# Optimization experiments

Hardware: AMD Instinct MI355X
Metric: run time of the kernel (lower is better)

Reference implementation:

```python
import jax, jax.numpy as jnp
import numpy as np

N_NODES = 65536
N_EDGES = 1048576
IN_F = 128
HID_F = 128
OUT_F = 128


def setup_inputs() -> dict:
    key = jax.random.key(0)
    ks = jax.random.split(key, 8)
    feat = jax.random.normal(ks[0], (N_NODES, IN_F), dtype=jnp.float32)
    eweight = jax.random.uniform(ks[1], (N_EDGES, 1), dtype=jnp.float32)
    W1 = jax.random.normal(ks[2], (IN_F, HID_F), dtype=jnp.float32) * (1.0 / np.sqrt(IN_F))
    b1 = jnp.zeros((HID_F,), dtype=jnp.float32)
    W2 = jax.random.normal(ks[3], (HID_F, OUT_F), dtype=jnp.float32) * (1.0 / np.sqrt(HID_F))
    b2 = jnp.zeros((OUT_F,), dtype=jnp.float32)
    src = jax.random.randint(ks[4], (N_EDGES,), 0, N_NODES, dtype=jnp.int32)
    dst = jax.random.randint(ks[5], (N_EDGES,), 0, N_NODES, dtype=jnp.int32)
    return {"feat": feat, "eweight": eweight, "W1": W1, "b1": b1,
            "W2": W2, "b2": b2, "src": src, "dst": dst}


def _degrees(src, dst, n_nodes):
    ones = jnp.ones(src.shape[0], dtype=jnp.float32)
    deg_out = jax.ops.segment_sum(ones, src, num_segments=n_nodes)
    deg_in = jax.ops.segment_sum(ones, dst, num_segments=n_nodes)
    # DGL GraphConv clamps degree to min 1 before norm='both'
    return jnp.clip(deg_out, 1.0, None), jnp.clip(deg_in, 1.0, None)


def _graph_conv(feat, W, b, src, dst, out_norm, in_norm, n_nodes):
    # DGL GraphConv, norm='both': D_out^{-1/2} x -> x W -> spmm sum -> D_in^{-1/2} -> + b
    h = feat * out_norm[:, None]
    h = h @ W
    agg = jax.ops.segment_sum(h[src], dst, num_segments=n_nodes)
    return agg * in_norm[:, None] + b


def reference(feat, eweight, W1, b1, W2, b2, src, dst):
    n = feat.shape[0]
    deg_out, deg_in = _degrees(src, dst, n)
    out_norm = jax.lax.rsqrt(deg_out)
    in_norm = jax.lax.rsqrt(deg_in)
    h = _graph_conv(feat, W1, b1, src, dst, out_norm, in_norm, n)
    h = jax.nn.relu(h)
    h = _graph_conv(h, W2, b2, src, dst, out_norm, in_norm, n)
    # final update_all: u_mul_e + sum (eweight given)
    msg = h[src] * eweight  # [E, OUT_F]
    return jax.ops.segment_sum(msg, dst, num_segments=n)
```

## Files before the change

### kernel.cpp

```cpp
#include <hip/hip_runtime.h>

#define F 128
#define NBA 512
#define COARSE 256
#define CAP_BIN 4864
#define CAP_CSR 5632

typedef unsigned int uint;
typedef unsigned short ushort;
typedef unsigned char uchar;
typedef __attribute__((ext_vector_type(8))) short short8;
typedef __attribute__((ext_vector_type(8))) unsigned short ushort8;
typedef __attribute__((ext_vector_type(4))) float floatx4;

__device__ __forceinline__ ushort f2bf(float f) {
  uint u = __float_as_uint(f);
  u += 0x7fffu + ((u >> 16) & 1u);
  return (ushort)(u >> 16);
}

__global__ __launch_bounds__(256) void w_prep(const float* __restrict__ W1,
                                              const float* __restrict__ W2,
                                              ushort* __restrict__ W1t,
                                              ushort* __restrict__ W2t) {
  int b = blockIdx.x;
  const float* W = (b < 64) ? W1 : W2;
  ushort* Wt = (b < 64) ? W1t : W2t;
  int idx = (b & 63) * 256 + threadIdx.x;
  int k = idx >> 7, n = idx & 127;
  Wt[n * F + k] = f2bf(W[idx]);
}

__global__ void init_cursors(int* __restrict__ cursorD, int* __restrict__ cursorS) {
  int t = threadIdx.x;
  cursorD[t] = t * CAP_BIN;
  cursorS[t] = t * CAP_BIN;
}

__global__ __launch_bounds__(256) void bin_edges(
    const int* __restrict__ src, const int* __restrict__ dst,
    const float* __restrict__ ew, int E,
    int* __restrict__ cursorD, int* __restrict__ cursorS,
    uchar* __restrict__ dstKeyF, uint* __restrict__ payload, uchar* __restrict__ srcF) {
  __shared__ int cnt[COARSE];
  __shared__ int base[COARSE];
  bool isD = blockIdx.x < NBA;
  int blk = isD ? blockIdx.x : blockIdx.x - NBA;
  const int* key = isD ? dst : src;
  int* cursor = isD ? cursorD : cursorS;
  if (threadIdx.x < COARSE) cnt[threadIdx.x] = 0;
  __syncthreads();
  int chunk = (E + NBA - 1) / NBA;
  int s0 = blk * chunk, s1 = min(E, s0 + chunk);
  for (int i = s0 + threadIdx.x; i < s1; i += 256)
    atomicAdd(&cnt[key[i] >> 8], 1);
  __syncthreads();
  if (threadIdx.x < COARSE) {
    int c = cnt[threadIdx.x];
    base[threadIdx.x] = c ? atomicAdd(&cursor[threadIdx.x], c) : 0;
    cnt[threadIdx.x] = 0;
  }
  __syncthreads();
  if (isD) {
    for (int i = s0 + threadIdx.x; i < s1; i += 256) {
      int d = dst[i];
      int bin = d >> 8;
      int p = base[bin] + atomicAdd(&cnt[bin], 1);
      if (p < (bin + 1) * CAP_BIN) {
        dstKeyF[p] = (uchar)(d & 255);
        payload[p] = (uint)(src[i] & 0xffff) | ((uint)f2bf(ew[i]) << 16);
      }
    }
  } else {
    for (int i = s0 + threadIdx.x; i < s1; i += 256) {
      int s = src[i];
      int bin = s >> 8;
      int p = base[bin] + atomicAdd(&cnt[bin], 1);
      if (p < (bin + 1) * CAP_BIN) srcF[p] = (uchar)(s & 255);
    }
  }
}

__global__ __launch_bounds__(1024) void bucket_csr(
    const uchar* __restrict__ dstKeyF, const uint* __restrict__ payload,
    const int* __restrict__ cursorD, int2* __restrict__ rowRange,
    float* __restrict__ inNorm, uint* __restrict__ csr,
    const uchar* __restrict__ srcF, const int* __restrict__ cursorS,
    float* __restrict__ outNorm) {
  __shared__ int hist[256], base[256], cur[256];
  int b = blockIdx.x, t = threadIdx.x;
  int lo = b * CAP_BIN;
  int cntD = min(cursorD[b] - lo, CAP_BIN);
  int hi = lo + cntD;
  if (t < 256) hist[t] = 0;
  __syncthreads();
  for (int i = lo + t; i < hi; i += 1024)
    atomicAdd(&hist[dstKeyF[i]], 1);
  __syncthreads();
  if (t < 256) base[t] = (hist[t] + 3) & ~3;
  __syncthreads();
  for (int off = 1; off < 256; off <<= 1) {
    int x = 0;
    if (t < 256 && t >= off) x = base[t - off];
    __syncthreads();
    if (t < 256) base[t] += x;
    __syncthreads();
  }
  if (t < 256) {
    int v = hist[t];
    int sz4 = (v + 3) & ~3;
    int st = b * CAP_CSR + base[t] - sz4;
    base[t] = st;
    cur[t] = 0;
    int node = b * 256 + t;
    rowRange[node] = make_int2(st, v);
    inNorm[node] = rsqrtf((float)max(v, 1));
  }
  __syncthreads();
  for (int i = lo + t; i < hi; i += 1024) {
    int fine = dstKeyF[i];
    int p = base[fine] + atomicAdd(&cur[fine], 1);
    csr[p] = payload[i];
  }
  __syncthreads();
  if (t < 256) hist[t] = 0;
  __syncthreads();
  int cntS = min(cursorS[b] - lo, CAP_BIN);
  for (int i = lo + t; i < lo + cntS; i += 1024)
    atomicAdd(&hist[srcF[i]], 1);
  __syncthreads();
  if (t < 256) outNorm[b * 256 + t] = rsqrtf((float)max(hist[t], 1));
}


template <bool BF16IN>
__global__ __launch_bounds__(256) void gemm_mfma(
    const void* __restrict__ Xv, const float* __restrict__ scale,
    const ushort* __restrict__ Wt, ushort* __restrict__ Y) {
  __shared__ ushort sA[128 * 136];
  __shared__ ushort sB[128 * 136];
  int t = threadIdx.x;
  int row0 = blockIdx.x * 128;

  {
    int r = t >> 1, hf = t & 1;
    ushort* ap = sA + r * 136 + hf * 64;
    if (BF16IN) {
      const ushort* xp = (const ushort*)Xv + (size_t)(row0 + r) * F + hf * 64;
#pragma unroll
      for (int j = 0; j < 8; ++j)
        *(ushort8*)(ap + j * 8) = *(const ushort8*)(xp + j * 8);
    } else {
      const float* xp = (const float*)Xv + (size_t)(row0 + r) * F + hf * 64;
      float s = scale[row0 + r];
#pragma unroll
      for (int j = 0; j < 8; ++j) {
        float4 v0 = *(const float4*)(xp + j * 8);
        float4 v1 = *(const float4*)(xp + j * 8 + 4);
        ushort8 o;
        o[0] = f2bf(v0.x * s); o[1] = f2bf(v0.y * s); o[2] = f2bf(v0.z * s); o[3] = f2bf(v0.w * s);
        o[4] = f2bf(v1.x * s); o[5] = f2bf(v1.y * s); o[6] = f2bf(v1.z * s); o[7] = f2bf(v1.w * s);
        *(ushort8*)(ap + j * 8) = o;
      }
    }
  }
  {
    int n = t >> 1, hf = t & 1;
    const ushort* wp = Wt + n * F + hf * 64;
    ushort* bp = sB + n * 136 + hf * 64;
#pragma unroll
    for (int j = 0; j < 8; ++j)
      *(ushort8*)(bp + j * 8) = *(const ushort8*)(wp + j * 8);
  }
  __syncthreads();

  int lane = t & 63, wave = t >> 6;
  int quad = lane >> 4, l16 = lane & 15;
  int mrow0 = wave * 32;

  floatx4 acc[2][8];
#pragma unroll
  for (int a = 0; a < 2; ++a)
#pragma unroll
    for (int c = 0; c < 8; ++c) acc[a][c] = (floatx4){0.f, 0.f, 0.f, 0.f};

#pragma unroll
  for (int kc = 0; kc < 128; kc += 32) {
    short8 afrag[2], bfrag[8];
#pragma unroll
    for (int a = 0; a < 2; ++a)
      afrag[a] = *(const short8*)(sA + (mrow0 + a * 16 + l16) * 136 + kc + quad * 8);
#pragma unroll
    for (int c = 0; c < 8; ++c)
      bfrag[c] = *(const short8*)(sB + (c * 16 + l16) * 136 + kc + quad * 8);
#pragma unroll
    for (int a = 0; a < 2; ++a)
#pragma unroll
      for (int c = 0; c < 8; ++c)
        acc[a][c] = __builtin_amdgcn_mfma_f32_16x16x32_bf16(afrag[a], bfrag[c], acc[a][c], 0, 0, 0);
  }

#pragma unroll
  for (int a = 0; a < 2; ++a)
#pragma unroll
    for (int c = 0; c < 8; ++c)
#pragma unroll
      for (int r = 0; r < 4; ++r) {
        int row = row0 + mrow0 + a * 16 + quad * 4 + r;
        int col = c * 16 + l16;
        Y[(size_t)row * F + col] = f2bf(acc[a][c][r]);
      }
}


template <bool EW, bool NB, bool RELU, bool PS, bool OUT_BF16>
__global__ __launch_bounds__(256) void spmm(
    const ushort* __restrict__ hb, const int2* __restrict__ rowRange,
    const uint* __restrict__ csr, const float* __restrict__ inNorm,
    const float* __restrict__ bias, const float* __restrict__ postScale,
    void* __restrict__ outv) {
  int node = blockIdx.x * 4 + (threadIdx.x >> 6);
  int lane = threadIdx.x & 63;
  int2 rr = rowRange[node];
  int base = rr.x, len = rr.y;

  float ax0 = 0.f, ay0 = 0.f, ax1 = 0.f, ay1 = 0.f;
  float ax2 = 0.f, ay2 = 0.f, ax3 = 0.f, ay3 = 0.f;
  int i = 0;
  for (; i + 8 <= len; i += 8) {
    uint4 c0 = *(const uint4*)(csr + base + i);
    uint4 c1 = *(const uint4*)(csr + base + i + 4);
    uint e0 = c0.x, e1 = c0.y, e2 = c0.z, e3 = c0.w;
    uint e4 = c1.x, e5 = c1.y, e6 = c1.z, e7 = c1.w;
    uint w0 = *((const uint*)(hb + ((size_t)(e0 & 0xffffu) << 7)) + lane);
    uint w1 = *((const uint*)(hb + ((size_t)(e1 & 0xffffu) << 7)) + lane);
    uint w2 = *((const uint*)(hb + ((size_t)(e2 & 0xffffu) << 7)) + lane);
    uint w3 = *((const uint*)(hb + ((size_t)(e3 & 0xffffu) << 7)) + lane);
    uint w4 = *((const uint*)(hb + ((size_t)(e4 & 0xffffu) << 7)) + lane);
    uint w5 = *((const uint*)(hb + ((size_t)(e5 & 0xffffu) << 7)) + lane);
    uint w6 = *((const uint*)(hb + ((size_t)(e6 & 0xffffu) << 7)) + lane);
    uint w7 = *((const uint*)(hb + ((size_t)(e7 & 0xffffu) << 7)) + lane);
    if (EW) {
      float q0 = __uint_as_float(e0 & 0xffff0000u), q1 = __uint_as_float(e1 & 0xffff0000u);
      float q2 = __uint_as_float(e2 & 0xffff0000u), q3 = __uint_as_float(e3 & 0xffff0000u);
      float q4 = __uint_as_float(e4 & 0xffff0000u), q5 = __uint_as_float(e5 & 0xffff0000u);
      float q6 = __uint_as_float(e6 & 0xffff0000u), q7 = __uint_as_float(e7 & 0xffff0000u);
      ax0 = fmaf(__uint_as_float(w0 << 16), q0, ax0); ay0 = fmaf(__uint_as_float(w0 & 0xffff0000u), q0, ay0);
      ax1 = fmaf(__uint_as_float(w1 << 16), q1, ax1); ay1 = fmaf(__uint_as_float(w1 & 0xffff0000u), q1, ay1);
      ax2 = fmaf(__uint_as_float(w2 << 16), q2, ax2); ay2 = fmaf(__uint_as_float(w2 & 0xffff0000u), q2, ay2);
      ax3 = fmaf(__uint_as_float(w3 << 16), q3, ax3); ay3 = fmaf(__uint_as_float(w3 & 0xffff0000u), q3, ay3);
      ax0 = fmaf(__uint_as_float(w4 << 16), q4, ax0); ay0 = fmaf(__uint_as_float(w4 & 0xffff0000u), q4, ay0);
      ax1 = fmaf(__uint_as_float(w5 << 16), q5, ax1); ay1 = fmaf(__uint_as_float(w5 & 0xffff0000u), q5, ay1);
      ax2 = fmaf(__uint_as_float(w6 << 16), q6, ax2); ay2 = fmaf(__uint_as_float(w6 & 0xffff0000u), q6, ay2);
      ax3 = fmaf(__uint_as_float(w7 << 16), q7, ax3); ay3 = fmaf(__uint_as_float(w7 & 0xffff0000u), q7, ay3);
    } else {
      ax0 += __uint_as_float(w0 << 16) + __uint_as_float(w4 << 16);
      ay0 += __uint_as_float(w0 & 0xffff0000u) + __uint_as_float(w4 & 0xffff0000u);
      ax1 += __uint_as_float(w1 << 16) + __uint_as_float(w5 << 16);
      ay1 += __uint_as_float(w1 & 0xffff0000u) + __uint_as_float(w5 & 0xffff0000u);
      ax2 += __uint_as_float(w2 << 16) + __uint_as_float(w6 << 16);
      ay2 += __uint_as_float(w2 & 0xffff0000u) + __uint_as_float(w6 & 0xffff0000u);
      ax3 += __uint_as_float(w3 << 16) + __uint_as_float(w7 << 16);
      ay3 += __uint_as_float(w3 & 0xffff0000u) + __uint_as_float(w7 & 0xffff0000u);
    }
  }
  if (i + 4 <= len) {
    uint4 c = *(const uint4*)(csr + base + i);
    uint e0 = c.x, e1 = c.y, e2 = c.z, e3 = c.w;
    uint w0 = *((const uint*)(hb + ((size_t)(e0 & 0xffffu) << 7)) + lane);
    uint w1 = *((const uint*)(hb + ((size_t)(e1 & 0xffffu) << 7)) + lane);
    uint w2 = *((const uint*)(hb + ((size_t)(e2 & 0xffffu) << 7)) + lane);
    uint w3 = *((const uint*)(hb + ((size_t)(e3 & 0xffffu) << 7)) + lane);
    float q0 = EW ? __uint_as_float(e0 & 0xffff0000u) : 1.f;
    float q1 = EW ? __uint_as_float(e1 & 0xffff0000u) : 1.f;
    float q2 = EW ? __uint_as_float(e2 & 0xffff0000u) : 1.f;
    float q3 = EW ? __uint_as_float(e3 & 0xffff0000u) : 1.f;
    ax0 = fmaf(__uint_as_float(w0 << 16), q0, ax0); ay0 = fmaf(__uint_as_float(w0 & 0xffff0000u), q0, ay0);
    ax1 = fmaf(__uint_as_float(w1 << 16), q1, ax1); ay1 = fmaf(__uint_as_float(w1 & 0xffff0000u), q1, ay1);
    ax2 = fmaf(__uint_as_float(w2 << 16), q2, ax2); ay2 = fmaf(__uint_as_float(w2 & 0xffff0000u), q2, ay2);
    ax3 = fmaf(__uint_as_float(w3 << 16), q3, ax3); ay3 = fmaf(__uint_as_float(w3 & 0xffff0000u), q3, ay3);
    i += 4;
  }
  int r = len - i;
  if (r > 0) {
    uint4 c = *(const uint4*)(csr + base + i);
    uint ee[4] = {c.x, c.y, c.z, c.w};
#pragma unroll
    for (int j = 0; j < 3; ++j) {
      if (j < r) {
        uint wj = *((const uint*)(hb + ((size_t)(ee[j] & 0xffffu) << 7)) + lane);
        float q = EW ? __uint_as_float(ee[j] & 0xffff0000u) : 1.f;
        if (j == 0) { ax0 = fmaf(__uint_as_float(wj << 16), q, ax0); ay0 = fmaf(__uint_as_float(wj & 0xffff0000u), q, ay0); }
        if (j == 1) { ax1 = fmaf(__uint_as_float(wj << 16), q, ax1); ay1 = fmaf(__uint_as_float(wj & 0xffff0000u), q, ay1); }
        if (j == 2) { ax2 = fmaf(__uint_as_float(wj << 16), q, ax2); ay2 = fmaf(__uint_as_float(wj & 0xffff0000u), q, ay2); }
      }
    }
  }
  float rx = (ax0 + ax1) + (ax2 + ax3);
  float ry = (ay0 + ay1) + (ay2 + ay3);
  if (NB) {
    float sc = inNorm[node];
    float2 b = *((const float2*)bias + lane);
    rx = fmaf(rx, sc, b.x);
    ry = fmaf(ry, sc, b.y);
    if (RELU) { rx = fmaxf(rx, 0.f); ry = fmaxf(ry, 0.f); }
    if (PS) { float o = postScale[node]; rx *= o; ry *= o; }
  }
  if (OUT_BF16) {
    uint p = ((uint)f2bf(ry) << 16) | (uint)f2bf(rx);
    *((uint*)outv + ((size_t)node << 6) + lane) = p;
  } else {
    float2 rv = {rx, ry};
    *((float2*)outv + ((size_t)node << 6) + lane) = rv;
  }
}


extern "C" void kernel_launch(void* const* d_in, const int* in_sizes, int n_in,
                              void* d_out, int out_size, void* d_ws, size_t ws_size,
                              hipStream_t stream) {
  const float* feat = (const float*)d_in[0];
  const float* ew   = (const float*)d_in[1];
  const float* W1   = (const float*)d_in[2];
  const float* b1   = (const float*)d_in[3];
  const float* W2   = (const float*)d_in[4];
  const float* b2   = (const float*)d_in[5];
  const int*   src  = (const int*)d_in[6];
  const int*   dst  = (const int*)d_in[7];
  const int N = in_sizes[0] / F;
  const int E = in_sizes[6];
  float* out = (float*)d_out;

  char* ws = (char*)d_ws;
  size_t off = 0;
  auto alloc = [&](size_t bytes) {
    void* p = ws + off;
    off += (bytes + 255) & ~(size_t)255;
    return p;
  };
  int2*   rowRange = (int2*)alloc((size_t)N * 8);
  float*  inNorm   = (float*)alloc((size_t)N * 4);
  float*  outNorm  = (float*)alloc((size_t)N * 4);
  ushort* W1t      = (ushort*)alloc((size_t)F * F * 2);
  ushort* W2t      = (ushort*)alloc((size_t)F * F * 2);
  int*    cursorD  = (int*)alloc(COARSE * 4);
  int*    cursorS  = (int*)alloc(COARSE * 4);
  uint*   csr      = (uint*)alloc((size_t)COARSE * CAP_CSR * 4);
  ushort* bufAb    = (ushort*)alloc((size_t)N * F * 2);
  ushort* bufBb    = (ushort*)alloc((size_t)N * F * 2);
  ushort* bufCb    = (ushort*)alloc((size_t)N * F * 2);
  if (off > ws_size) return;

  uint*  payload;
  uchar* dstKeyF;
  uchar* srcF;
  {
    char* tp = (char*)bufBb;
    size_t toff = 0;
    auto talloc = [&](size_t bytes) {
      void* p = tp + toff;
      toff += (bytes + 255) & ~(size_t)255;
      return p;
    };
    payload = (uint*)talloc((size_t)COARSE * CAP_BIN * 4);
    dstKeyF = (uchar*)talloc((size_t)COARSE * CAP_BIN);
    srcF    = (uchar*)talloc((size_t)COARSE * CAP_BIN);
  }

  w_prep<<<128, 256, 0, stream>>>(W1, W2, W1t, W2t);
  init_cursors<<<1, COARSE, 0, stream>>>(cursorD, cursorS);
  bin_edges<<<2 * NBA, 256, 0, stream>>>(src, dst, ew, E, cursorD, cursorS,
                                         dstKeyF, payload, srcF);
  bucket_csr<<<COARSE, 1024, 0, stream>>>(dstKeyF, payload, cursorD,
                                          rowRange, inNorm, csr,
                                          srcF, cursorS, outNorm);

  gemm_mfma<false><<<N / 128, 256, 0, stream>>>(feat, outNorm, W1t, bufAb);
  spmm<false, true, true, true, true><<<N / 4, 256, 0, stream>>>(
      bufAb, rowRange, csr, inNorm, b1, outNorm, bufBb);
  gemm_mfma<true><<<N / 128, 256, 0, stream>>>(bufBb, nullptr, W2t, bufAb);
  spmm<false, true, false, false, true><<<N / 4, 256, 0, stream>>>(
      bufAb, rowRange, csr, inNorm, b2, nullptr, bufCb);
  spmm<true, false, false, false, false><<<N / 4, 256, 0, stream>>>(
      bufCb, rowRange, csr, nullptr, nullptr, nullptr, out);
}
```

Before: 277.5 us.

## Restructure edge binning: per-wave histograms, packed slots, split norm blocks

Edge binning now keeps a separate shared-memory histogram per wave to reduce atomic contention. It uses fewer blocks for the source-degree pass and packs the dst key and payload into a single uint2 slot, so bucket_csr does one coalesced read per edge. The out-degree histogram moves into its own set of bucket_csr blocks so it runs in parallel with CSR construction instead of after it. Cursors are zeroed with hipMemsetAsync and become offsets relative to each bin, which replaces the init kernel. The cost is wider 8-byte slots, which raise scratch traffic during binning.

```diff
diff --git a/kernel.cpp b/kernel.cpp
--- a/kernel.cpp
+++ b/kernel.cpp
@@ -2,6 +2,7 @@
 
 #define F 128
 #define NBA 512
+#define NBS 128
 #define COARSE 256
 #define CAP_BIN 4864
 #define CAP_CSR 5632
@@ -31,71 +32,82 @@
   Wt[n * F + k] = f2bf(W[idx]);
 }
 
-__global__ void init_cursors(int* __restrict__ cursorD, int* __restrict__ cursorS) {
-  int t = threadIdx.x;
-  cursorD[t] = t * CAP_BIN;
-  cursorS[t] = t * CAP_BIN;
-}
-
 __global__ __launch_bounds__(256) void bin_edges(
     const int* __restrict__ src, const int* __restrict__ dst,
     const float* __restrict__ ew, int E,
     int* __restrict__ cursorD, int* __restrict__ cursorS,
-    uchar* __restrict__ dstKeyF, uint* __restrict__ payload, uchar* __restrict__ srcF) {
-  __shared__ int cnt[COARSE];
+    uint2* __restrict__ slotD, uchar* __restrict__ srcF) {
+  __shared__ int cnt[4][COARSE];
   __shared__ int base[COARSE];
   bool isD = blockIdx.x < NBA;
   int blk = isD ? blockIdx.x : blockIdx.x - NBA;
+  int nblk = isD ? NBA : NBS;
   const int* key = isD ? dst : src;
   int* cursor = isD ? cursorD : cursorS;
-  if (threadIdx.x < COARSE) cnt[threadIdx.x] = 0;
-  __syncthreads();
-  int chunk = (E + NBA - 1) / NBA;
+  int wave = threadIdx.x >> 6;
+  for (int i = threadIdx.x; i < 4 * COARSE; i += 256) ((int*)cnt)[i] = 0;
+  __syncthreads();
+  int chunk = (E + nblk - 1) / nblk;
   int s0 = blk * chunk, s1 = min(E, s0 + chunk);
   for (int i = s0 + threadIdx.x; i < s1; i += 256)
-    atomicAdd(&cnt[key[i] >> 8], 1);
+    atomicAdd(&cnt[wave][key[i] >> 8], 1);
   __syncthreads();
   if (threadIdx.x < COARSE) {
-    int c = cnt[threadIdx.x];
-    base[threadIdx.x] = c ? atomicAdd(&cursor[threadIdx.x], c) : 0;
-    cnt[threadIdx.x] = 0;
+    int b = threadIdx.x;
+    int tot = cnt[0][b] + cnt[1][b] + cnt[2][b] + cnt[3][b];
+    base[b] = tot ? atomicAdd(&cursor[b], tot) : 0;
+    cnt[0][b] = 0;
   }
   __syncthreads();
   if (isD) {
     for (int i = s0 + threadIdx.x; i < s1; i += 256) {
       int d = dst[i];
       int bin = d >> 8;
-      int p = base[bin] + atomicAdd(&cnt[bin], 1);
-      if (p < (bin + 1) * CAP_BIN) {
-        dstKeyF[p] = (uchar)(d & 255);
-        payload[p] = (uint)(src[i] & 0xffff) | ((uint)f2bf(ew[i]) << 16);
+      int p = base[bin] + atomicAdd(&cnt[0][bin], 1);
+      if (p < CAP_BIN) {
+        uint2 v;
+        v.x = (uint)(src[i] & 0xffff) | ((uint)f2bf(ew[i]) << 16);
+        v.y = (uint)(d & 255);
+        slotD[(size_t)bin * CAP_BIN + p] = v;
       }
     }
   } else {
     for (int i = s0 + threadIdx.x; i < s1; i += 256) {
       int s = src[i];
       int bin = s >> 8;
-      int p = base[bin] + atomicAdd(&cnt[bin], 1);
-      if (p < (bin + 1) * CAP_BIN) srcF[p] = (uchar)(s & 255);
+      int p = base[bin] + atomicAdd(&cnt[0][bin], 1);
+      if (p < CAP_BIN) srcF[(size_t)bin * CAP_BIN + p] = (uchar)(s & 255);
     }
   }
 }
 
 __global__ __launch_bounds__(1024) void bucket_csr(
-    const uchar* __restrict__ dstKeyF, const uint* __restrict__ payload,
-    const int* __restrict__ cursorD, int2* __restrict__ rowRange,
-    float* __restrict__ inNorm, uint* __restrict__ csr,
+    const uint2* __restrict__ slotD, const int* __restrict__ cursorD,
+    int2* __restrict__ rowRange, float* __restrict__ inNorm, uint* __restrict__ csr,
     const uchar* __restrict__ srcF, const int* __restrict__ cursorS,
     float* __restrict__ outNorm) {
   __shared__ int hist[256], base[256], cur[256];
-  int b = blockIdx.x, t = threadIdx.x;
+  int t = threadIdx.x;
+  if (blockIdx.x >= COARSE) {
+    int b = blockIdx.x - COARSE;
+    int lo = b * CAP_BIN;
+    int cntS = min(cursorS[b], CAP_BIN);
+    if (t < 256) hist[t] = 0;
+    __syncthreads();
+    for (int i = lo + t; i < lo + cntS; i += 1024)
+      atomicAdd(&hist[srcF[i]], 1);
+    __syncthreads();
+    if (t < 256) outNorm[b * 256 + t] = rsqrtf((float)max(hist[t], 1));
+    return;
+  }
+  int b = blockIdx.x;
   int lo = b * CAP_BIN;
-  int cntD = min(cursorD[b] - lo, CAP_BIN);
+  int cntD = min(cursorD[b], CAP_BIN);
   int hi = lo + cntD;
   if (t < 256) hist[t] = 0;
   __syncthreads();
   for (int i = lo + t; i < hi; i += 1024)
-    atomicAdd(&hist[dstKeyF[i]], 1);
+    atomicAdd(&hist[slotD[i].y], 1);
   __syncthreads();
   if (t < 256) base[t] = (hist[t] + 3) & ~3;
   __syncthreads();
@@ -118,18 +130,11 @@
   }
   __syncthreads();
   for (int i = lo + t; i < hi; i += 1024) {
-    int fine = dstKeyF[i];
+    uint2 v = slotD[i];
+    int fine = v.y;
     int p = base[fine] + atomicAdd(&cur[fine], 1);
-    csr[p] = payload[i];
-  }
-  __syncthreads();
-  if (t < 256) hist[t] = 0;
-  __syncthreads();
-  int cntS = min(cursorS[b] - lo, CAP_BIN);
-  for (int i = lo + t; i < lo + cntS; i += 1024)
-    atomicAdd(&hist[srcF[i]], 1);
-  __syncthreads();
-  if (t < 256) outNorm[b * 256 + t] = rsqrtf((float)max(hist[t], 1));
+    csr[p] = v.x;
+  }
 }
 
 
@@ -351,8 +356,7 @@
   ushort* bufCb    = (ushort*)alloc((size_t)N * F * 2);
   if (off > ws_size) return;
 
-  uint*  payload;
-  uchar* dstKeyF;
+  uint2* slotD;
   uchar* srcF;
   {
     char* tp = (char*)bufBb;
@@ -362,18 +366,15 @@
       toff += (bytes + 255) & ~(size_t)255;
       return p;
     };
-    payload = (uint*)talloc((size_t)COARSE * CAP_BIN * 4);
-    dstKeyF = (uchar*)talloc((size_t)COARSE * CAP_BIN);
-    srcF    = (uchar*)talloc((size_t)COARSE * CAP_BIN);
-  }
-
+    slotD = (uint2*)talloc((size_t)COARSE * CAP_BIN * 8);
+    srcF  = (uchar*)talloc((size_t)COARSE * CAP_BIN);
+  }
+
+  hipMemsetAsync(cursorD, 0, 2 * COARSE * 4, stream);
   w_prep<<<128, 256, 0, stream>>>(W1, W2, W1t, W2t);
-  init_cursors<<<1, COARSE, 0, stream>>>(cursorD, cursorS);
-  bin_edges<<<2 * NBA, 256, 0, stream>>>(src, dst, ew, E, cursorD, cursorS,
-                                         dstKeyF, payload, srcF);
-  bucket_csr<<<COARSE, 1024, 0, stream>>>(dstKeyF, payload, cursorD,
-                                          rowRange, inNorm, csr,
-                                          srcF, cursorS, outNorm);
+  bin_edges<<<NBA + NBS, 256, 0, stream>>>(src, dst, ew, E, cursorD, cursorS, slotD, srcF);
+  bucket_csr<<<2 * COARSE, 1024, 0, stream>>>(slotD, cursorD, rowRange, inNorm, csr,
+                                              srcF, cursorS, outNorm);
 
   gemm_mfma<false><<<N / 128, 256, 0, stream>>>(feat, outNorm, W1t, bufAb);
   spmm<false, true, true, true, true><<<N / 4, 256, 0, stream>>>(
```

Result: no change. 281.8 us (+1.6%).
